# Performance work log

Hardware: AMD Instinct MI355X
Metric: run time of the kernel (lower is better)

The kernel has to match this reference:

```python
import jax, jax.numpy as jnp
import numpy as np

B, T, D_MODEL, N_HEADS = 2, 2048, 1024, 16
HEAD_DIM = D_MODEL // N_HEADS


def _ln(x, g, b, eps=1e-5):
    m = x.mean(-1, keepdims=True)
    v = ((x - m) ** 2).mean(-1, keepdims=True)
    return (x - m) / jnp.sqrt(v + eps) * g + b


def setup_inputs() -> dict:
    key = jax.random.key(0)
    ks = jax.random.split(key, 7)
    f = jnp.float32
    x = jax.random.normal(ks[0], (B, T, D_MODEL), f)
    Wq = jax.random.normal(ks[1], (D_MODEL, D_MODEL), f) * 0.02
    Wk = jax.random.normal(ks[2], (D_MODEL, D_MODEL), f) * 0.02
    Wv = jax.random.normal(ks[3], (D_MODEL, D_MODEL), f) * 0.02
    Wo = jax.random.normal(ks[4], (D_MODEL, D_MODEL), f) * 0.02
    return {
        'x': x, 'Wq': Wq, 'Wk': Wk, 'Wv': Wv, 'Wo': Wo,
        'evolution_rate': jnp.asarray(0.1, f),
        'memory_decay': jnp.asarray(0.85, f),
        'temporal_weights': jax.random.normal(ks[5], (HEAD_DIM,), f) * 0.02,
        'q_gamma': jnp.ones((HEAD_DIM,), f), 'q_beta': jnp.zeros((HEAD_DIM,), f),
        'k_gamma': jnp.ones((HEAD_DIM,), f), 'k_beta': jnp.zeros((HEAD_DIM,), f),
    }


def reference(x, Wq, Wk, Wv, Wo, evolution_rate, memory_decay,
              temporal_weights, q_gamma, q_beta, k_gamma, k_beta):
    b, t, c = x.shape
    h, d = N_HEADS, HEAD_DIM
    # projections (torch Linear: y = x @ W^T), split heads -> [B,H,T,D]
    q = jnp.einsum('btc,oc->bto', x, Wq).reshape(b, t, h, d).transpose(0, 2, 1, 3)
    k = jnp.einsum('btc,oc->bto', x, Wk).reshape(b, t, h, d).transpose(0, 2, 1, 3)
    v = jnp.einsum('btc,oc->bto', x, Wv).reshape(b, t, h, d).transpose(0, 2, 1, 3)

    sig_md = jax.nn.sigmoid(memory_decay)
    # temporal signal per position: sin(sigmoid(er)*(pos+1) * w)  -> [T,D]
    ef = jax.nn.sigmoid(evolution_rate) * jnp.arange(1, t + 1, dtype=x.dtype)
    ts = jnp.sin(ef[:, None] * temporal_weights[None, :])

    def step(mem, inp):  # mem: [B,H,D]
        q_t, k_t, ts_t = inp  # [B,H,D],[B,H,D],[D]
        eq = _ln(q_t + ts_t + sig_md * mem, q_gamma, q_beta)
        ek = _ln(k_t + 0.5 * ts_t + 0.3 * sig_md * mem, k_gamma, k_beta)
        return 0.7 * mem + 0.3 * q_t, (eq, ek)

    mem0 = jnp.zeros((b, h, d), x.dtype)
    qT = q.transpose(2, 0, 1, 3)  # [T,B,H,D]
    kT = k.transpose(2, 0, 1, 3)
    _, (eqT, ekT) = jax.lax.scan(step, mem0, (qT, kT, ts))
    eq = eqT.transpose(1, 2, 0, 3)  # [B,H,T,D]
    ek = ekT.transpose(1, 2, 0, 3)

    scale = 1.0 / np.sqrt(d).astype(np.float32)
    scores = jnp.einsum('bhtd,bhsd->bhts', eq, ek) * scale
    causal = jnp.tril(jnp.ones((t, t), bool))
    scores = jnp.where(causal[None, None], scores, -jnp.inf)
    w = jax.nn.softmax(scores, axis=-1)  # dropout is identity (eval)
    out = jnp.einsum('bhts,bhsd->bhtd', w, v)
    out = out.transpose(0, 2, 1, 3).reshape(b, t, c)
    return jnp.einsum('btc,oc->bto', out, Wo)
```

## Files before the change

### kernel.cpp

```cpp
#include <hip/hip_runtime.h>
#include <stdint.h>

#define T_SEQ   2048
#define NHEADS  16
#define HDIM    64
#define DMODEL  1024

typedef __attribute__((ext_vector_type(8))) _Float16 half8_t;
typedef __attribute__((ext_vector_type(4))) float    float4_t;

typedef __attribute__((address_space(1))) unsigned char ga_u8;
typedef __attribute__((address_space(3))) unsigned char lds_u8;

__device__ __forceinline__ unsigned short f2h(float f) {
  _Float16 h = (_Float16)f;
  return __builtin_bit_cast(unsigned short, h);
}
__device__ __forceinline__ float h2f(unsigned short u) {
  return (float)__builtin_bit_cast(_Float16, u);
}
__device__ __forceinline__ unsigned packh2(float a, float b) {
  return (unsigned)f2h(a) | ((unsigned)f2h(b) << 16);
}
__device__ __forceinline__ unsigned packu2(unsigned short a, unsigned short b) {
  return (unsigned)a | ((unsigned)b << 16);
}
__device__ __forceinline__ void async_copy16(const void* g, void* l) {
  __builtin_amdgcn_global_load_lds((ga_u8*)g, (lds_u8*)l, 16, 0, 0);
}

__global__ __launch_bounds__(256) void cvt_f32_f16(const float* __restrict__ s,
                                                   unsigned short* __restrict__ d, int n4) {
  int i = blockIdx.x * 256 + threadIdx.x;
  if (i >= n4) return;
  float4 v = ((const float4*)s)[i];
  ushort4 o;
  o.x = f2h(v.x); o.y = f2h(v.y); o.z = f2h(v.z); o.w = f2h(v.w);
  ((ushort4*)d)[i] = o;
}

__global__ __launch_bounds__(256) void cvt_weights(
    const float* __restrict__ w0, const float* __restrict__ w1,
    const float* __restrict__ w2, const float* __restrict__ w3,
    unsigned short* __restrict__ d0, unsigned short* __restrict__ d1,
    unsigned short* __restrict__ d2, unsigned short* __restrict__ d3, int n4) {
  int i = blockIdx.x * 256 + threadIdx.x;
  if (i >= n4) return;
  const float* s = (blockIdx.y == 0) ? w0 : (blockIdx.y == 1) ? w1 : (blockIdx.y == 2) ? w2 : w3;
  unsigned short* d = (blockIdx.y == 0) ? d0 : (blockIdx.y == 1) ? d1 : (blockIdx.y == 2) ? d2 : d3;
  float4 v = ((const float4*)s)[i];
  ushort4 o;
  o.x = f2h(v.x); o.y = f2h(v.y); o.z = f2h(v.z); o.w = f2h(v.w);
  ((ushort4*)d)[i] = o;
}

__global__ __launch_bounds__(256) void gemm_qkv(
    const unsigned short* __restrict__ A,
    const unsigned short* __restrict__ Bq, const unsigned short* __restrict__ Bk,
    const unsigned short* __restrict__ Bv,
    unsigned short* __restrict__ Cq, unsigned short* __restrict__ Ck,
    unsigned short* __restrict__ Cv) {
  const unsigned short* B = (blockIdx.z == 0) ? Bq : (blockIdx.z == 1) ? Bk : Bv;
  unsigned short*       C = (blockIdx.z == 0) ? Cq : (blockIdx.z == 1) ? Ck : Cv;

  __shared__ alignas(16) unsigned short As[128 * 32];
  __shared__ alignas(16) unsigned short Bs[128 * 32];
  const int tid  = threadIdx.x;
  const int lane = tid & 63, w = tid >> 6;
  const int c = lane & 15, g = lane >> 4;
  const int wr = w >> 1, wc = w & 1;
  const int m0 = blockIdx.y * 128, n0 = blockIdx.x * 128;

  float4_t acc[4][4];
#pragma unroll
  for (int m = 0; m < 4; ++m)
#pragma unroll
    for (int n = 0; n < 4; ++n) acc[m][n] = (float4_t){0.f, 0.f, 0.f, 0.f};

  for (int k0 = 0; k0 < 1024; k0 += 32) {
    __syncthreads();
#pragma unroll
    for (int r = 0; r < 2; ++r) {
      const int idx = r * 256 + tid;
      const int row = idx >> 2, kc = (idx & 3) * 8;
      async_copy16(A + (size_t)(m0 + row) * 1024 + k0 + kc, As + r * 2048 + w * 512);
      async_copy16(B + (size_t)(n0 + row) * 1024 + k0 + kc, Bs + r * 2048 + w * 512);
    }
    __syncthreads();
    half8_t af[4], bf[4];
#pragma unroll
    for (int m = 0; m < 4; ++m) af[m] = *(const half8_t*)&As[(wr * 64 + m * 16 + c) * 32 + g * 8];
#pragma unroll
    for (int n = 0; n < 4; ++n) bf[n] = *(const half8_t*)&Bs[(wc * 64 + n * 16 + c) * 32 + g * 8];
#pragma unroll
    for (int m = 0; m < 4; ++m)
#pragma unroll
      for (int n = 0; n < 4; ++n)
        acc[m][n] = __builtin_amdgcn_mfma_f32_16x16x32_f16(af[m], bf[n], acc[m][n], 0, 0, 0);
  }
#pragma unroll
  for (int m = 0; m < 4; ++m)
#pragma unroll
    for (int j = 0; j < 4; ++j) {
      const int row = m0 + wr * 64 + m * 16 + g * 4 + j;
#pragma unroll
      for (int n = 0; n < 4; ++n) {
        const int col = n0 + wc * 64 + n * 16 + c;
        C[(size_t)row * 1024 + col] = f2h(acc[m][n][j]);
      }
    }
}

__global__ __launch_bounds__(256) void gemm_nt_out(const unsigned short* __restrict__ A,
                                                   const unsigned short* __restrict__ B,
                                                   float* __restrict__ C) {
  __shared__ alignas(16) unsigned short As[128 * 32];
  __shared__ alignas(16) unsigned short Bs[128 * 32];
  const int tid  = threadIdx.x;
  const int lane = tid & 63, w = tid >> 6;
  const int c = lane & 15, g = lane >> 4;
  const int wr = w >> 1, wc = w & 1;
  const int m0 = blockIdx.y * 128, n0 = blockIdx.x * 128;

  float4_t acc[4][4];
#pragma unroll
  for (int m = 0; m < 4; ++m)
#pragma unroll
    for (int n = 0; n < 4; ++n) acc[m][n] = (float4_t){0.f, 0.f, 0.f, 0.f};

  for (int k0 = 0; k0 < 1024; k0 += 32) {
    __syncthreads();
#pragma unroll
    for (int r = 0; r < 2; ++r) {
      const int idx = r * 256 + tid;
      const int row = idx >> 2, kc = (idx & 3) * 8;
      async_copy16(A + (size_t)(m0 + row) * 1024 + k0 + kc, As + r * 2048 + w * 512);
      async_copy16(B + (size_t)(n0 + row) * 1024 + k0 + kc, Bs + r * 2048 + w * 512);
    }
    __syncthreads();
    half8_t af[4], bf[4];
#pragma unroll
    for (int m = 0; m < 4; ++m) af[m] = *(const half8_t*)&As[(wr * 64 + m * 16 + c) * 32 + g * 8];
#pragma unroll
    for (int n = 0; n < 4; ++n) bf[n] = *(const half8_t*)&Bs[(wc * 64 + n * 16 + c) * 32 + g * 8];
#pragma unroll
    for (int m = 0; m < 4; ++m)
#pragma unroll
      for (int n = 0; n < 4; ++n)
        acc[m][n] = __builtin_amdgcn_mfma_f32_16x16x32_f16(af[m], bf[n], acc[m][n], 0, 0, 0);
  }
#pragma unroll
  for (int m = 0; m < 4; ++m)
#pragma unroll
    for (int j = 0; j < 4; ++j) {
      const int row = m0 + wr * 64 + m * 16 + g * 4 + j;
#pragma unroll
      for (int n = 0; n < 4; ++n) {
        const int col = n0 + wc * 64 + n * 16 + c;
        C[(size_t)row * 1024 + col] = acc[m][n][j];
      }
    }
}

__global__ __launch_bounds__(64) void evolve_ln(
    const unsigned short* __restrict__ q, const unsigned short* __restrict__ k,
    const float* __restrict__ er_p, const float* __restrict__ md_p,
    const float* __restrict__ tw, const float* __restrict__ qgamma,
    const float* __restrict__ qbeta, const float* __restrict__ kgamma,
    const float* __restrict__ kbeta,
    unsigned short* __restrict__ eq, unsigned short* __restrict__ ek) {
  const int lane = threadIdx.x;
  const int t0 = blockIdx.x * 32;
  const int bh = blockIdx.y;
  const int b = bh >> 4, h = bh & 15;
  const float sig_er = 1.f / (1.f + expf(-er_p[0]));
  const float smd    = 1.f / (1.f + expf(-md_p[0]));
  const float wv = tw[lane];
  const float gq = qgamma[lane], bq = qbeta[lane];
  const float gk = kgamma[lane], bk = kbeta[lane];
  const size_t base = ((size_t)b * T_SEQ) * DMODEL + h * HDIM + lane;

  float mem = 0.f;
  const int start = (t0 >= 64) ? (t0 - 64) : 0;
  for (int t = start; t < t0; ++t)
    mem = 0.7f * mem + 0.3f * h2f(q[base + (size_t)t * DMODEL]);

  for (int t = t0; t < t0 + 32; ++t) {
    const float qv = h2f(q[base + (size_t)t * DMODEL]);
    const float kv = h2f(k[base + (size_t)t * DMODEL]);
    const float ts = sinf(sig_er * (float)(t + 1) * wv);
    const float xq = qv + ts + smd * mem;
    const float xk = kv + 0.5f * ts + 0.3f * smd * mem;
    float s1 = xq, s2 = xq * xq, s3 = xk, s4 = xk * xk;
#pragma unroll
    for (int off = 32; off > 0; off >>= 1) {
      s1 += __shfl_xor(s1, off);
      s2 += __shfl_xor(s2, off);
      s3 += __shfl_xor(s3, off);
      s4 += __shfl_xor(s4, off);
    }
    const float mq = s1 * (1.f / 64.f);
    const float vq = fmaxf(s2 * (1.f / 64.f) - mq * mq, 0.f);
    const float mk = s3 * (1.f / 64.f);
    const float vk = fmaxf(s4 * (1.f / 64.f) - mk * mk, 0.f);
    eq[base + (size_t)t * DMODEL] = f2h((xq - mq) * rsqrtf(vq + 1e-5f) * gq + bq);
    ek[base + (size_t)t * DMODEL] = f2h((xk - mk) * rsqrtf(vk + 1e-5f) * gk + bk);
    mem = 0.7f * mem + 0.3f * qv;
  }
}

__global__ __launch_bounds__(256) void attn_fused(
    const unsigned short* __restrict__ eq, const unsigned short* __restrict__ ek,
    const unsigned short* __restrict__ v, unsigned short* __restrict__ o) {
  __shared__ alignas(16) float Ssh[4][16][36];
  __shared__ float Alds[4][16];
  __shared__ float Llds[4][16];
  const int tid = threadIdx.x;
  const int lane = tid & 63, w = tid >> 6;
  const int c = lane & 15, g = lane >> 4;
  const int p = blockIdx.x * 4 + w;
  const int bh = blockIdx.y;
  const int b = bh >> 4, h = bh & 15;
  const size_t head = ((size_t)b * T_SEQ) * DMODEL + h * HDIM;

  for (int half = 0; half < 2; ++half) {
    const int sub = half ? (127 - p) : p;
    const int qw = sub * 16;
    const int qrow = qw + c;

    const half8_t aq0 = *(const half8_t*)(eq + head + (size_t)qrow * DMODEL + g * 8);
    const half8_t aq1 = *(const half8_t*)(eq + head + (size_t)qrow * DMODEL + 32 + g * 8);

    float4_t acc[4];
#pragma unroll
    for (int n = 0; n < 4; ++n) acc[n] = (float4_t){0.f, 0.f, 0.f, 0.f};
    float mrun = -1e30f, lsum = 0.f;

    const int ntiles = (qw >> 5) + 1;
    for (int tile = 0; tile < ntiles; ++tile) {
      const int s0 = tile * 32;
#pragma unroll
      for (int st = 0; st < 2; ++st) {
        const unsigned short* ekr = ek + head + (size_t)(s0 + st * 16 + c) * DMODEL;
        const half8_t bk0 = *(const half8_t*)(ekr + g * 8);
        const half8_t bk1 = *(const half8_t*)(ekr + 32 + g * 8);
        float4_t z = (float4_t){0.f, 0.f, 0.f, 0.f};
        z = __builtin_amdgcn_mfma_f32_16x16x32_f16(aq0, bk0, z, 0, 0, 0);
        z = __builtin_amdgcn_mfma_f32_16x16x32_f16(aq1, bk1, z, 0, 0, 0);
#pragma unroll
        for (int j = 0; j < 4; ++j)
          Ssh[w][g * 4 + j][st * 16 + c] = z[j] * 0.125f;
      }

      float pf[8];
      float tmax = -1e30f;
#pragma unroll
      for (int e = 0; e < 8; ++e) {
        const int sa = s0 + g * 8 + e;
        const float val = (sa <= qrow) ? Ssh[w][c][g * 8 + e] : -1e30f;
        pf[e] = val;
        tmax = fmaxf(tmax, val);
      }
      tmax = fmaxf(tmax, __shfl_xor(tmax, 16));
      tmax = fmaxf(tmax, __shfl_xor(tmax, 32));
      const float mnew = fmaxf(mrun, tmax);
      const float alpha = __expf(mrun - mnew);
      mrun = mnew;
      float psum = 0.f;
#pragma unroll
      for (int e = 0; e < 8; ++e) {
        pf[e] = __expf(pf[e] - mnew);
        psum += pf[e];
      }
      psum += __shfl_xor(psum, 16);
      psum += __shfl_xor(psum, 32);
      lsum = lsum * alpha + psum;
      if (g == 0) Alds[w][c] = alpha;

      uint4 pu;
      pu.x = packh2(pf[0], pf[1]);
      pu.y = packh2(pf[2], pf[3]);
      pu.z = packh2(pf[4], pf[5]);
      pu.w = packh2(pf[6], pf[7]);
      const half8_t pa = __builtin_bit_cast(half8_t, pu);

      float af[4];
#pragma unroll
      for (int j = 0; j < 4; ++j) af[j] = Alds[w][g * 4 + j];
#pragma unroll
      for (int n = 0; n < 4; ++n) {
        acc[n][0] *= af[0]; acc[n][1] *= af[1];
        acc[n][2] *= af[2]; acc[n][3] *= af[3];
      }
      const unsigned short* vp = v + head + (size_t)(s0 + g * 8) * DMODEL + c;
#pragma unroll
      for (int n = 0; n < 4; ++n) {
        const unsigned short* vq2 = vp + n * 16;
        uint4 bu;
        bu.x = packu2(vq2[0 * DMODEL], vq2[1 * DMODEL]);
        bu.y = packu2(vq2[2 * DMODEL], vq2[3 * DMODEL]);
        bu.z = packu2(vq2[4 * DMODEL], vq2[5 * DMODEL]);
        bu.w = packu2(vq2[6 * DMODEL], vq2[7 * DMODEL]);
        const half8_t bv = __builtin_bit_cast(half8_t, bu);
        acc[n] = __builtin_amdgcn_mfma_f32_16x16x32_f16(pa, bv, acc[n], 0, 0, 0);
      }
    }

    if (g == 0) Llds[w][c] = lsum;
    float lj[4];
#pragma unroll
    for (int j = 0; j < 4; ++j) lj[j] = 1.f / Llds[w][g * 4 + j];
#pragma unroll
    for (int n = 0; n < 4; ++n)
#pragma unroll
      for (int j = 0; j < 4; ++j)
        o[head + (size_t)(qw + g * 4 + j) * DMODEL + n * 16 + c] = f2h(acc[n][j] * lj[j]);
  }
}

extern "C" void kernel_launch(void* const* d_in, const int* in_sizes, int n_in,
                              void* d_out, int out_size, void* d_ws, size_t ws_size,
                              hipStream_t stream) {
  const float* x  = (const float*)d_in[0];
  const float* Wq = (const float*)d_in[1];
  const float* Wk = (const float*)d_in[2];
  const float* Wv = (const float*)d_in[3];
  const float* Wo = (const float*)d_in[4];
  const float* er = (const float*)d_in[5];
  const float* md = (const float*)d_in[6];
  const float* tw = (const float*)d_in[7];
  const float* qg = (const float*)d_in[8];
  const float* qb = (const float*)d_in[9];
  const float* kg = (const float*)d_in[10];
  const float* kb = (const float*)d_in[11];

  const size_t NX = (size_t)2 * T_SEQ * DMODEL;
  const size_t NW = (size_t)DMODEL * DMODEL;

  unsigned short* xh  = (unsigned short*)d_ws;
  unsigned short* woh = xh + NX;
  unsigned short* wqh = woh + NW;
  unsigned short* wkh = wqh + NW;
  unsigned short* wvh = wkh + NW;
  unsigned short* qh  = wvh + NW;
  unsigned short* kh  = qh + NX;
  unsigned short* vh  = kh + NX;
  unsigned short* ekh = vh + NX;
  unsigned short* aoh = ekh + NX;
  unsigned short* eqh = xh;

  const int n4x = (int)(NX / 4), n4w = (int)(NW / 4);

  cvt_f32_f16<<<n4x / 256, 256, 0, stream>>>(x, xh, n4x);
  cvt_weights<<<dim3(n4w / 256, 4), 256, 0, stream>>>(Wq, Wk, Wv, Wo,
                                                      wqh, wkh, wvh, woh, n4w);

  gemm_qkv<<<dim3(8, 32, 3), 256, 0, stream>>>(xh, wqh, wkh, wvh, qh, kh, vh);

  evolve_ln<<<dim3(T_SEQ / 32, 32), 64, 0, stream>>>(qh, kh, er, md, tw,
                                                     qg, qb, kg, kb, eqh, ekh);

  attn_fused<<<dim3(16, 32), 256, 0, stream>>>(eqh, ekh, vh, aoh);

  gemm_nt_out<<<dim3(8, 32), 256, 0, stream>>>(aoh, woh, (float*)d_out);
}
```

Before: 213.8 us.

## Split attention KV range in two and merge partials in combine kernel

Splits each query block's causal key range into two halves handled by separate blocks (split-K / flash-decoding style), doubling the attention grid to 1024 blocks. Each half writes normalized fp16 partial outputs plus (max, sum) stats, and a new combine kernel rescales and merges them. The aim is better occupancy and load balance across CUs, at the cost of an extra kernel launch, extra global traffic for partials, and fp16 rounding of partial outputs. Partials reuse the q buffer region, which is dead after evolve_ln.

```diff
diff --git a/kernel.cpp b/kernel.cpp
--- a/kernel.cpp
+++ b/kernel.cpp
@@ -209,19 +209,22 @@
   }
 }
 
-__global__ __launch_bounds__(256) void attn_fused(
+__global__ __launch_bounds__(256) void attn_split(
     const unsigned short* __restrict__ eq, const unsigned short* __restrict__ ek,
-    const unsigned short* __restrict__ v, unsigned short* __restrict__ o) {
+    const unsigned short* __restrict__ v, unsigned short* __restrict__ opart,
+    float2* __restrict__ ml) {
   __shared__ alignas(16) float Ssh[4][16][36];
   __shared__ float Alds[4][16];
   __shared__ float Llds[4][16];
   const int tid = threadIdx.x;
   const int lane = tid & 63, w = tid >> 6;
   const int c = lane & 15, g = lane >> 4;
-  const int p = blockIdx.x * 4 + w;
+  const int pg = blockIdx.x & 15, kh = blockIdx.x >> 4;
+  const int p = pg * 4 + w;
   const int bh = blockIdx.y;
   const int b = bh >> 4, h = bh & 15;
   const size_t head = ((size_t)b * T_SEQ) * DMODEL + h * HDIM;
+  const size_t pbase = (size_t)kh * ((size_t)2 * T_SEQ * DMODEL);
 
   for (int half = 0; half < 2; ++half) {
     const int sub = half ? (127 - p) : p;
@@ -237,7 +240,10 @@
     float mrun = -1e30f, lsum = 0.f;
 
     const int ntiles = (qw >> 5) + 1;
-    for (int tile = 0; tile < ntiles; ++tile) {
+    const int h1 = (ntiles + 1) >> 1;
+    const int t_lo = kh ? h1 : 0;
+    const int t_hi = kh ? ntiles : h1;
+    for (int tile = t_lo; tile < t_hi; ++tile) {
       const int s0 = tile * 32;
 #pragma unroll
       for (int st = 0; st < 2; ++st) {
@@ -306,16 +312,59 @@
       }
     }
 
-    if (g == 0) Llds[w][c] = lsum;
+    if (g == 0) {
+      Llds[w][c] = lsum;
+      ml[(size_t)kh * (32 * T_SEQ) + (size_t)bh * T_SEQ + qw + c] = make_float2(mrun, lsum);
+    }
     float lj[4];
 #pragma unroll
-    for (int j = 0; j < 4; ++j) lj[j] = 1.f / Llds[w][g * 4 + j];
+    for (int j = 0; j < 4; ++j) {
+      const float lv = Llds[w][g * 4 + j];
+      lj[j] = (lv > 0.f) ? 1.f / lv : 0.f;
+    }
 #pragma unroll
     for (int n = 0; n < 4; ++n)
 #pragma unroll
       for (int j = 0; j < 4; ++j)
-        o[head + (size_t)(qw + g * 4 + j) * DMODEL + n * 16 + c] = f2h(acc[n][j] * lj[j]);
+        opart[pbase + head + (size_t)(qw + g * 4 + j) * DMODEL + n * 16 + c] =
+            f2h(acc[n][j] * lj[j]);
   }
+}
+
+__global__ __launch_bounds__(256) void attn_combine(
+    const unsigned short* __restrict__ opart, const float2* __restrict__ ml,
+    unsigned short* __restrict__ o) {
+  const int g8 = blockIdx.x * 256 + threadIdx.x;
+  const size_t e0 = (size_t)g8 * 8;
+  const int b = (int)(e0 >> 21);
+  const int t = (int)((e0 >> 10) & 2047);
+  const int h = ((int)e0 & 1023) >> 6;
+  const int mli = ((b * NHEADS + h) << 11) | t;
+
+  const float2 p1 = ml[mli];
+  const float2 p2 = ml[32 * T_SEQ + mli];
+  const float mm = fmaxf(p1.x, p2.x);
+  const float w1 = p1.y * __expf(p1.x - mm);
+  const float w2 = p2.y * __expf(p2.x - mm);
+  const float inv = 1.f / (w1 + w2);
+  const float c1 = w1 * inv, c2 = w2 * inv;
+
+  const uint4 u1 = *(const uint4*)(opart + e0);
+  const uint4 u2 = *(const uint4*)(opart + (size_t)2 * T_SEQ * DMODEL + e0);
+  uint4 r;
+  unsigned ua[4] = {u1.x, u1.y, u1.z, u1.w};
+  unsigned ub[4] = {u2.x, u2.y, u2.z, u2.w};
+  unsigned ro[4];
+#pragma unroll
+  for (int i = 0; i < 4; ++i) {
+    const float a0 = h2f((unsigned short)(ua[i] & 0xffffu));
+    const float a1 = h2f((unsigned short)(ua[i] >> 16));
+    const float b0 = h2f((unsigned short)(ub[i] & 0xffffu));
+    const float b1 = h2f((unsigned short)(ub[i] >> 16));
+    ro[i] = packh2(c1 * a0 + c2 * b0, c1 * a1 + c2 * b1);
+  }
+  r.x = ro[0]; r.y = ro[1]; r.z = ro[2]; r.w = ro[3];
+  *(uint4*)(o + e0) = r;
 }
 
 extern "C" void kernel_launch(void* const* d_in, const int* in_sizes, int n_in,
@@ -347,7 +396,9 @@
   unsigned short* vh  = kh + NX;
   unsigned short* ekh = vh + NX;
   unsigned short* aoh = ekh + NX;
+  float2*         ml  = (float2*)(aoh + NX);
   unsigned short* eqh = xh;
+  unsigned short* opart = qh;
 
   const int n4x = (int)(NX / 4), n4w = (int)(NW / 4);
 
@@ -360,7 +411,8 @@
   evolve_ln<<<dim3(T_SEQ / 32, 32), 64, 0, stream>>>(qh, kh, er, md, tw,
                                                      qg, qb, kg, kb, eqh, ekh);
 
-  attn_fused<<<dim3(16, 32), 256, 0, stream>>>(eqh, ekh, vh, aoh);
+  attn_split<<<dim3(32, 32), 256, 0, stream>>>(eqh, ekh, vh, opart, ml);
+  attn_combine<<<(int)(NX / 8 / 256), 256, 0, stream>>>(opart, ml, aoh);
 
   gemm_nt_out<<<dim3(8, 32), 256, 0, stream>>>(aoh, woh, (float*)d_out);
 }
```

Result: slower. 237.6 us (+11.1%).
